# Kernel optimization log

Measured on AMD Instinct MI355X. Metric: run time of the kernel, lower is better.

## Reference

```python
import jax, jax.numpy as jnp
import numpy as np
from jax import lax

NC = 80
REG_MAX = 16
BINS = REG_MAX + 1
RADIUS = 2.5
TOPK = 10
L_BOX, L_CLS, L_DFL = 7.5, 1.0, 1.5


def focal_bce(x, t, alpha=0.25, gamma=2.0):
    # numerically stable BCE-with-logits: max(x,0) - x*t + log1p(exp(-|x|))
    p = jax.nn.sigmoid(x)
    ce = jnp.maximum(x, 0.0) - x * t + jnp.log1p(jnp.exp(-jnp.abs(x)))
    p_t = p * t + (1.0 - p) * (1.0 - t)
    a_t = alpha * t + (1.0 - alpha) * (1.0 - t)
    return ce * a_t * (1.0 - p_t) ** gamma


def _level_loss(reg, cls, boxes, labels, stride):
    B, _, H, W = reg.shape
    HW = H * W
    G = boxes.shape[1]
    gy, gx = jnp.meshgrid(jnp.arange(H, dtype=jnp.float32), jnp.arange(W, dtype=jnp.float32), indexing='ij')
    centers = jnp.stack([gx + 0.5, gy + 0.5], -1).reshape(HW, 2)  # [HW,2]
    gt = boxes / stride  # [B,G,4]
    gctr = (gt[..., :2] + gt[..., 2:]) * 0.5  # [B,G,2]
    cx = centers[None, :, None, 0]
    cy = centers[None, :, None, 1]
    dl = cx - gt[:, None, :, 0]
    dt = cy - gt[:, None, :, 1]
    dr = gt[:, None, :, 2] - cx
    db = gt[:, None, :, 3] - cy
    in_gt = (dl > 0) & (dt > 0) & (dr > 0) & (db > 0)
    in_ctr = ((cx >= gctr[:, None, :, 0] - RADIUS) & (cx <= gctr[:, None, :, 0] + RADIUS)
              & (cy >= gctr[:, None, :, 1] - RADIUS) & (cy <= gctr[:, None, :, 1] + RADIUS))
    mask = in_gt & in_ctr  # [B,HW,G]
    any_pos = jnp.any(mask, axis=(1, 2))  # [B]
    # fallback: topk closest anchor centers per GT (smallest distance along point dim)
    dist = jnp.sqrt(((centers[None, :, None, :] - gctr[:, None, :, :]) ** 2).sum(-1))  # [B,HW,G]
    k = min(TOPK, HW)
    _, idx = lax.top_k(-jnp.swapaxes(dist, 1, 2), k)  # [B,G,k]
    fb = jnp.zeros((B, HW, G), bool).at[jnp.arange(B)[:, None, None], idx, jnp.arange(G)[None, :, None]].set(True)
    mask = jnp.where(any_pos[:, None, None], mask, fb)
    mf = mask.astype(jnp.float32)
    n_pos = mf.sum((1, 2))  # [B] (>=1 by construction of fallback)

    cls_flat = cls.transpose(0, 2, 3, 1).reshape(B, HW, NC)
    reg_flat = reg.transpose(0, 2, 3, 1).reshape(B, HW, 4, BINS)

    # ---- DFL ----
    ltrb = jnp.clip(jnp.stack([dl, dt, dr, db], -1), 0.0)  # [B,HW,G,4]
    tgt = jnp.clip(ltrb, 0.0, REG_MAX - 1e-4)
    lb = jnp.floor(tgt).astype(jnp.int32)
    rb = jnp.minimum(lb + 1, REG_MAX)
    wl = rb.astype(jnp.float32) - tgt
    wr = tgt - lb.astype(jnp.float32)
    logp = jax.nn.log_softmax(reg_flat, -1)  # [B,HW,4,BINS]
    bi = jnp.arange(B)[:, None, None, None]
    pi = jnp.arange(HW)[None, :, None, None]
    ki = jnp.arange(4)[None, None, None, :]
    dfl_pair = -(logp[bi, pi, ki, lb] * wl + logp[bi, pi, ki, rb] * wr)  # [B,HW,G,4]
    dfl = ((dfl_pair * mf[..., None]).sum((1, 2, 3)) / (n_pos * 4.0)).sum()

    # ---- box (IoU, detached as in original) ----
    prob = jax.nn.softmax(reg_flat, -1)
    d = (prob * jnp.arange(BINS, dtype=jnp.float32)).sum(-1)  # [B,HW,4]
    pcx = centers[None, :, 0]
    pcy = centers[None, :, 1]
    pred_box = jnp.stack([pcx - d[..., 0], pcy - d[..., 1], pcx + d[..., 2], pcy + d[..., 3]], -1)  # [B,HW,4]
    b1 = pred_box[:, :, None, :]
    b2 = gt[:, None, :, :]
    iw = jnp.clip(jnp.minimum(b1[..., 2:], b2[..., 2:]) - jnp.maximum(b1[..., :2], b2[..., :2]), 0.0)
    inter = iw[..., 0] * iw[..., 1]
    a1 = (b1[..., 2] - b1[..., 0]) * (b1[..., 3] - b1[..., 1])
    a2 = (b2[..., 2] - b2[..., 0]) * (b2[..., 3] - b2[..., 1])
    iou = lax.stop_gradient(inter / (a1 + a2 - inter + 1e-6))  # [B,HW,G]
    box = ((1.0 - iou) * mf).sum()

    # ---- cls (focal BCE, soft IoU targets). Decompose one-hot target:
    # per positive pair: sum_c f(logit_c,0) - f(logit_cls,0) + f(logit_cls,iou)
    fz = focal_bce(cls_flat, 0.0)  # [B,HW,NC]
    fz_sum = fz.sum(-1)  # [B,HW]
    bi2 = jnp.arange(B)[:, None, None]
    pi2 = jnp.arange(HW)[None, :, None]
    ci = labels[:, None, :]  # [B,1,G]
    cls_at = cls_flat[bi2, pi2, ci]  # [B,HW,G]
    fz_at = fz[bi2, pi2, ci]
    cls_pos = ((fz_sum[:, :, None] - fz_at + focal_bce(cls_at, iou)) * mf).sum()
    pos_pt = jnp.any(mask, -1)  # [B,HW]
    cls_neg = jnp.where(pos_pt, 0.0, fz_sum).sum()
    return box, cls_pos + cls_neg, dfl


def _total(reg0, cls0, reg1, cls1, reg2, cls2, gt_boxes, gt_labels):
    tb = tc = td = 0.0
    for r, c, s in ((reg0, cls0, 8.0), (reg1, cls1, 16.0), (reg2, cls2, 32.0)):
        b, cl, d = _level_loss(r, c, gt_boxes, gt_labels, s)
        tb = tb + b
        tc = tc + cl
        td = td + d
    loss = L_BOX * tb + L_CLS * tc + L_DFL * td
    return loss, tb, tc, td


def setup_inputs() -> dict:
    key = jax.random.key(0)
    ks = jax.random.split(key, 10)
    B, G = 16, 32
    d = {}
    for i, (h, w) in enumerate(((80, 80), (40, 40), (20, 20))):
        d[f'reg{i}'] = jax.random.normal(ks[2 * i], (B, 4 * BINS, h, w), jnp.float32)
        d[f'cls{i}'] = jax.random.normal(ks[2 * i + 1], (B, NC, h, w), jnp.float32)
    ctr = jax.random.uniform(ks[6], (B, G, 2), minval=0.0, maxval=640.0)
    wh = jax.random.uniform(ks[7], (B, G, 2), minval=16.0, maxval=160.0)
    x1y1 = jnp.clip(ctr - wh * 0.5, 0.0, 640.0)
    x2y2 = jnp.clip(ctr + wh * 0.5, 0.0, 640.0)
    d['gt_boxes'] = jnp.concatenate([x1y1, x2y2], -1)
    d['gt_labels'] = jax.random.randint(ks[8], (B, G), 0, NC, jnp.int32)
    return d


def reference(reg0, cls0, reg1, cls1, reg2, cls2, gt_boxes, gt_labels):
    return _total(reg0, cls0, reg1, cls1, reg2, cls2, gt_boxes, gt_labels)
```

## Files before the change

### kernel.cpp

```cpp
#include <hip/hip_runtime.h>
#include <math.h>

#define NCLS 80
#define BINS 17
#define REGMAX 16
#define NG 32
#define NB 16
#define KTOP 10
#define RAD 2.5f

#define PLANE    134400
#define FZP_OFF  256
#define DV_OFF   (256 + 8 * PLANE)
#define LZ_OFF   (256 + 12 * PLANE)
#define WS_NEED  ((size_t)(256 + 16 * PLANE) * 4)
#define NBLOCKS_B (34 * 16)

__device__ __constant__ int c_lvlbase[3] = { 0, 102400, 128000 };

__device__ __forceinline__ float focal0(float x) {
    float e   = __expf(-fabsf(x));
    float inv = 1.0f / (1.0f + e);
    float p   = (x >= 0.0f) ? inv : e * inv;
    float ce  = fmaxf(x, 0.0f) + __logf(1.0f + e);
    return ce * 0.75f * p * p;
}

__device__ __forceinline__ float focal_t(float x, float t) {
    float e   = __expf(-fabsf(x));
    float inv = 1.0f / (1.0f + e);
    float p   = (x >= 0.0f) ? inv : e * inv;
    float ce  = fmaxf(x, 0.0f) - x * t + __logf(1.0f + e);
    float pt  = p * t + (1.0f - p) * (1.0f - t);
    float at  = 0.25f * t + 0.75f * (1.0f - t);
    float om  = 1.0f - pt;
    return ce * at * om * om;
}

__global__ __launch_bounds__(512) void k_stream(
    const float* __restrict__ reg0, const float* __restrict__ cls0,
    const float* __restrict__ reg1, const float* __restrict__ cls1,
    const float* __restrict__ reg2, const float* __restrict__ cls2,
    float* __restrict__ ws)
{
    int id  = blockIdx.x;
    int tid = threadIdx.x;
    if (id < 192) {
        int lvl = id / 64, rem = id % 64, b = rem / 4, k = rem % 4;
        const float* regp = (lvl == 0) ? reg0 : (lvl == 1 ? reg1 : reg2);
        int W  = (lvl == 0) ? 80 : (lvl == 1 ? 40 : 20);
        int HW = W * W;
        const float* base = regp + (size_t)(b * 68 + k * BINS) * HW;
        float sm[16], ex[16];
#pragma unroll
        for (int i = 0; i < 16; ++i) { sm[i] = 0.f; ex[i] = 0.f; }
        for (int t = 0; t < BINS; ++t) {
            const float* rb = base + (size_t)t * HW;
            float tf = (float)t;
#pragma unroll
            for (int j = 0; j < 4; ++j) {
                int p = tid * 4 + 2048 * j;
                if (p < HW) {
                    float4 x = *(const float4*)(rb + p);
                    float e0 = __expf(x.x), e1 = __expf(x.y);
                    float e2 = __expf(x.z), e3 = __expf(x.w);
                    sm[j*4+0] += e0; ex[j*4+0] += e0 * tf;
                    sm[j*4+1] += e1; ex[j*4+1] += e1 * tf;
                    sm[j*4+2] += e2; ex[j*4+2] += e2 * tf;
                    sm[j*4+3] += e3; ex[j*4+3] += e3 * tf;
                }
            }
        }
        int pidx = c_lvlbase[lvl] + b * HW;
#pragma unroll
        for (int j = 0; j < 4; ++j) {
            int p = tid * 4 + 2048 * j;
            if (p < HW) {
                float4 dv4 = make_float4(ex[j*4+0] / sm[j*4+0], ex[j*4+1] / sm[j*4+1],
                                         ex[j*4+2] / sm[j*4+2], ex[j*4+3] / sm[j*4+3]);
                float4 lz4 = make_float4(__logf(sm[j*4+0]), __logf(sm[j*4+1]),
                                         __logf(sm[j*4+2]), __logf(sm[j*4+3]));
                *(float4*)(ws + DV_OFF + (size_t)k * PLANE + pidx + p) = dv4;
                *(float4*)(ws + LZ_OFF + (size_t)k * PLANE + pidx + p) = lz4;
            }
        }
    } else {
        int id2 = id - 192;
        int lvl = id2 / 128, rem = id2 % 128, b = rem / 8, cg = rem % 8;
        const float* clsp = (lvl == 0) ? cls0 : (lvl == 1 ? cls1 : cls2);
        int W  = (lvl == 0) ? 80 : (lvl == 1 ? 40 : 20);
        int HW = W * W;
        const float* base = clsp + (size_t)(b * 80 + cg * 10) * HW;
        float fz[16];
#pragma unroll
        for (int i = 0; i < 16; ++i) fz[i] = 0.f;
        for (int t = 0; t < 10; ++t) {
            const float* rb = base + (size_t)t * HW;
#pragma unroll
            for (int j = 0; j < 4; ++j) {
                int p = tid * 4 + 2048 * j;
                if (p < HW) {
                    float4 x = *(const float4*)(rb + p);
                    fz[j*4+0] += focal0(x.x); fz[j*4+1] += focal0(x.y);
                    fz[j*4+2] += focal0(x.z); fz[j*4+3] += focal0(x.w);
                }
            }
        }
        int pidx = c_lvlbase[lvl] + b * HW;
#pragma unroll
        for (int j = 0; j < 4; ++j) {
            int p = tid * 4 + 2048 * j;
            if (p < HW) {
                *(float4*)(ws + FZP_OFF + (size_t)cg * PLANE + pidx + p) =
                    make_float4(fz[j*4+0], fz[j*4+1], fz[j*4+2], fz[j*4+3]);
            }
        }
    }
}

__global__ __launch_bounds__(256) void k_finish(
    const float* __restrict__ reg0, const float* __restrict__ cls0,
    const float* __restrict__ reg1, const float* __restrict__ cls1,
    const float* __restrict__ reg2, const float* __restrict__ cls2,
    const float* __restrict__ gtb,  const int* __restrict__ lab,
    float* __restrict__ ws, float* __restrict__ out)
{
    float* acc  = ws;
    float* npos = ws + 8;
    float* dfln = ws + 56;
    int*   cnt  = (int*)(ws + 152);

    int bx = blockIdx.x;
    int b  = blockIdx.y;
    int lvl, tix, W; const float *regp, *clsp; float inv_s;
    if (bx < 25)      { lvl = 0; tix = bx;      W = 80; regp = reg0; clsp = cls0; inv_s = 0.125f;   }
    else if (bx < 32) { lvl = 1; tix = bx - 25; W = 40; regp = reg1; clsp = cls1; inv_s = 0.0625f;  }
    else              { lvl = 2; tix = bx - 32; W = 20; regp = reg2; clsp = cls2; inv_s = 0.03125f; }
    int HW = W * W;
    int tile = tix * 256;

    int tid  = threadIdx.x;
    int lane = tid & 63;
    int w    = tid >> 6;
    int pt   = tile + tid;
    bool v   = pt < HW;
    int pidx = c_lvlbase[lvl] + b * HW + (v ? pt : 0);

    __shared__ float s_bx[NG][6];
    __shared__ int   s_lab[NG];
    __shared__ int   s_any, s_tick, s_fb[NG][KTOP];
    __shared__ float red[4][4];

    if (tid == 0) s_any = 0;
    if (tid < NG) {
        int g = tid;
        float4 bb4 = *(const float4*)(gtb + (b * NG + g) * 4);
        float x1 = bb4.x * inv_s, y1 = bb4.y * inv_s;
        float x2 = bb4.z * inv_s, y2 = bb4.w * inv_s;
        s_bx[g][0] = x1; s_bx[g][1] = y1; s_bx[g][2] = x2; s_bx[g][3] = y2;
        s_bx[g][4] = (x1 + x2) * 0.5f; s_bx[g][5] = (y1 + y2) * 0.5f;
        s_lab[g] = lab[b * NG + g];
    }
    __syncthreads();

    {
        int g = tid >> 3, wi = tid & 7;
        float x1 = s_bx[g][0], y1 = s_bx[g][1];
        float x2 = s_bx[g][2], y2 = s_bx[g][3];
        float gcx = s_bx[g][4], gcy = s_bx[g][5];
        int jc = (int)floorf(gcx), ic = (int)floorf(gcy);
        bool any = false;
#pragma unroll
        for (int r = 0; r < 11; ++r) {
            int ci = wi + 8 * r;
            if (ci < 81) {
                int j = jc + (ci % 9) - 4, i = ic + (ci / 9) - 4;
                if (j >= 0 && j < W && i >= 0 && i < W) {
                    float cx = (float)j + 0.5f, cy = (float)i + 0.5f;
                    bool m = (cx - x1 > 0.0f) && (cy - y1 > 0.0f) &&
                             (x2 - cx > 0.0f) && (y2 - cy > 0.0f) &&
                             (cx >= gcx - RAD) && (cx <= gcx + RAD) &&
                             (cy >= gcy - RAD) && (cy <= gcy + RAD);
                    any = any || m;
                }
            }
        }
        if (__any(any) && lane == 0) atomicOr(&s_any, 1);
    }
    __syncthreads();
    bool anyb = s_any != 0;

    if (!anyb) {
        if (tid < NG) {
            int g = tid;
            float gcx = s_bx[g][4], gcy = s_bx[g][5];
            float bd[KTOP]; int bi[KTOP];
            for (int t = 0; t < KTOP; ++t) { bd[t] = 3.0e38f; bi[t] = 0; }
            for (int p = 0; p < HW; ++p) {
                float cx = (float)(p % W) + 0.5f;
                float cy = (float)(p / W) + 0.5f;
                float dx = cx - gcx, dy = cy - gcy;
                float d = dx * dx + dy * dy;
                if (d < bd[KTOP - 1]) {
                    int t = KTOP - 1;
                    while (t > 0 && d < bd[t - 1]) { bd[t] = bd[t-1]; bi[t] = bi[t-1]; --t; }
                    bd[t] = d; bi[t] = p;
                }
            }
            for (int t = 0; t < KTOP; ++t) s_fb[g][t] = bi[t];
        }
        __syncthreads();
    }

    float fz = 0.f;
    if (v) {
#pragma unroll
        for (int cg = 0; cg < 8; ++cg)
            fz += ws[FZP_OFF + (size_t)cg * PLANE + pidx];
    }

    float bxa = 0.f, cla = 0.f, dfa = 0.f, np = 0.f;
    bool pos = false, ld = false;
    float dv0 = 0, dv1 = 0, dv2 = 0, dv3 = 0, lzv[4] = {0, 0, 0, 0};
    int ri = v ? pt / W : 0;
    float cy = (float)ri + 0.5f;
    float cx = (float)(pt - ri * W) + 0.5f;

    if (v) {
        for (int g = 0; g < NG; ++g) {
            float x1 = s_bx[g][0], y1 = s_bx[g][1];
            float x2 = s_bx[g][2], y2 = s_bx[g][3];
            float dl = cx - x1, dt = cy - y1, dr = x2 - cx, db = y2 - cy;
            bool mk;
            if (anyb) {
                float gx = s_bx[g][4], gy = s_bx[g][5];
                mk = (dl > 0.f) && (dt > 0.f) && (dr > 0.f) && (db > 0.f) &&
                     (cx >= gx - RAD) && (cx <= gx + RAD) &&
                     (cy >= gy - RAD) && (cy <= gy + RAD);
            } else {
                mk = false;
                for (int t = 0; t < KTOP; ++t) mk = mk || (s_fb[g][t] == pt);
            }
            if (mk) {
                pos = true;
                np += 1.f;
                if (!ld) {
                    dv0 = ws[DV_OFF + 0 * PLANE + pidx];
                    dv1 = ws[DV_OFF + 1 * PLANE + pidx];
                    dv2 = ws[DV_OFF + 2 * PLANE + pidx];
                    dv3 = ws[DV_OFF + 3 * PLANE + pidx];
#pragma unroll
                    for (int k = 0; k < 4; ++k)
                        lzv[k] = ws[LZ_OFF + (size_t)k * PLANE + pidx];
                    ld = true;
                }
                float px1 = cx - dv0, py1 = cy - dv1;
                float px2 = cx + dv2, py2 = cy + dv3;
                float pa = (px2 - px1) * (py2 - py1);
                float ix1 = fmaxf(px1, x1), iy1 = fmaxf(py1, y1);
                float ix2 = fminf(px2, x2), iy2 = fminf(py2, y2);
                float iw = fmaxf(ix2 - ix1, 0.f), ih = fmaxf(iy2 - iy1, 0.f);
                float inter = iw * ih;
                float ga = (x2 - x1) * (y2 - y1);
                float iou = inter / (pa + ga - inter + 1e-6f);
                bxa += 1.f - iou;
                float ltrb[4] = { dl, dt, dr, db };
#pragma unroll
                for (int k = 0; k < 4; ++k) {
                    float tt = fminf(fmaxf(ltrb[k], 0.f), 15.9999f);
                    float lf = floorf(tt); int lb = (int)lf;
                    int rb = lb + 1 > REGMAX ? REGMAX : lb + 1;
                    float wl = (float)rb - tt, wr = tt - lf;
                    float xl = regp[(size_t)(b * 68 + k * BINS + lb) * HW + pt];
                    float xr = regp[(size_t)(b * 68 + k * BINS + rb) * HW + pt];
                    dfa -= (xl - lzv[k]) * wl + (xr - lzv[k]) * wr;
                }
                int cc = s_lab[g];
                float xat = clsp[(size_t)(b * 80 + cc) * HW + pt];
                cla += fz - focal0(xat) + focal_t(xat, iou);
            }
        }
        if (!pos) cla += fz;
    }

    float v0 = bxa, v1 = cla, v2 = dfa, v3 = np;
    for (int off = 32; off > 0; off >>= 1) {
        v0 += __shfl_down(v0, off);
        v1 += __shfl_down(v1, off);
        v2 += __shfl_down(v2, off);
        v3 += __shfl_down(v3, off);
    }
    if (lane == 0) { red[w][0] = v0; red[w][1] = v1; red[w][2] = v2; red[w][3] = v3; }
    __syncthreads();
    if (tid == 0) {
        float t0 = 0, t1 = 0, t2 = 0, t3 = 0;
        for (int wv = 0; wv < 4; ++wv) {
            t0 += red[wv][0]; t1 += red[wv][1]; t2 += red[wv][2]; t3 += red[wv][3];
        }
        atomicAdd(&acc[0], t0);
        atomicAdd(&acc[1], t1);
        atomicAdd(&dfln[lvl * NB + b], t2);
        atomicAdd(&npos[lvl * NB + b], t3);
    }

    if (tid == 0) {
        __threadfence();
        s_tick = atomicAdd(cnt, 1);
    }
    __syncthreads();
    if (s_tick == NBLOCKS_B - 1 && tid < 64) {
        float vs = 0.f;
        if (lane < 48) {
            float n = atomicAdd(&npos[lane], 0.0f);
            float d = atomicAdd(&dfln[lane], 0.0f);
            if (n > 0.f) vs = d / (n * 4.0f);
        }
        for (int off = 32; off > 0; off >>= 1) vs += __shfl_down(vs, off);
        if (lane == 0) {
            float tbv = atomicAdd(&acc[0], 0.0f);
            float tcv = atomicAdd(&acc[1], 0.0f);
            out[0] = 7.5f * tbv + tcv + 1.5f * vs;
            out[1] = tbv; out[2] = tcv; out[3] = vs;
        }
    }
}

__global__ __launch_bounds__(512, 2) void k_main_fb(
    const float* __restrict__ reg0, const float* __restrict__ cls0,
    const float* __restrict__ reg1, const float* __restrict__ cls1,
    const float* __restrict__ reg2, const float* __restrict__ cls2,
    const float* __restrict__ gtb,  const int* __restrict__ lab,
    float* __restrict__ acc, float* __restrict__ npos, float* __restrict__ dfln,
    int* __restrict__ cnt, float* __restrict__ out)
{
    int bx = blockIdx.x;
    int b  = blockIdx.y;
    int lvl, tix, W; const float *regp, *clsp; float inv_s;
    if (bx < 25)      { lvl = 0; tix = bx;      W = 80; regp = reg0; clsp = cls0; inv_s = 0.125f;   }
    else if (bx < 32) { lvl = 1; tix = bx - 25; W = 40; regp = reg1; clsp = cls1; inv_s = 0.0625f;  }
    else              { lvl = 2; tix = bx - 32; W = 20; regp = reg2; clsp = cls2; inv_s = 0.03125f; }
    int HW = W * W;
    int tile = tix * 256;
    int tid  = threadIdx.x;
    int lane = tid & 63;
    int w    = tid >> 6;
    int p0   = tile + 4 * lane;
    bool v   = p0 < HW;
    int pb   = v ? p0 : HW - 4;

    __shared__ float s_bx[NG][6];
    __shared__ int   s_lab[NG];
    __shared__ float s_dv[4][256], s_lz[4][256], s_fzp[4][256], s_fzs[256];
    __shared__ unsigned char s_ps[8][64];
    __shared__ float red[8][4];
    __shared__ int   s_any, s_tick, s_fb[NG][KTOP];

    if (tid == 0) s_any = 0;
    if (tid < NG) {
        int g = tid;
        float4 bb4 = *(const float4*)(gtb + (b * NG + g) * 4);
        float x1 = bb4.x * inv_s, y1 = bb4.y * inv_s;
        float x2 = bb4.z * inv_s, y2 = bb4.w * inv_s;
        s_bx[g][0] = x1; s_bx[g][1] = y1; s_bx[g][2] = x2; s_bx[g][3] = y2;
        s_bx[g][4] = (x1 + x2) * 0.5f; s_bx[g][5] = (y1 + y2) * 0.5f;
        s_lab[g] = lab[b * NG + g];
    }
    __syncthreads();
    {
        int g = tid >> 4, wi = tid & 15;
        float x1 = s_bx[g][0], y1 = s_bx[g][1];
        float x2 = s_bx[g][2], y2 = s_bx[g][3];
        float gcx = s_bx[g][4], gcy = s_bx[g][5];
        int jc = (int)floorf(gcx), ic = (int)floorf(gcy);
        bool any = false;
#pragma unroll
        for (int r = 0; r < 6; ++r) {
            int ci = wi + 16 * r;
            if (ci < 81) {
                int j = jc + (ci % 9) - 4, i = ic + (ci / 9) - 4;
                if (j >= 0 && j < W && i >= 0 && i < W) {
                    float cx = (float)j + 0.5f, cy = (float)i + 0.5f;
                    bool m = (cx - x1 > 0.0f) && (cy - y1 > 0.0f) &&
                             (x2 - cx > 0.0f) && (y2 - cy > 0.0f) &&
                             (cx >= gcx - RAD) && (cx <= gcx + RAD) &&
                             (cy >= gcy - RAD) && (cy <= gcy + RAD);
                    any = any || m;
                }
            }
        }
        if (__any(any) && lane == 0) atomicOr(&s_any, 1);
    }
    __syncthreads();
    bool anyb = s_any != 0;
    if (!anyb) {
        if (tid < NG) {
            int g = tid;
            float gcx = s_bx[g][4], gcy = s_bx[g][5];
            float bd[KTOP]; int bi[KTOP];
            for (int t = 0; t < KTOP; ++t) { bd[t] = 3.0e38f; bi[t] = 0; }
            for (int p = 0; p < HW; ++p) {
                float cx = (float)(p % W) + 0.5f;
                float cy = (float)(p / W) + 0.5f;
                float dx = cx - gcx, dy = cy - gcy;
                float d = dx * dx + dy * dy;
                if (d < bd[KTOP - 1]) {
                    int t = KTOP - 1;
                    while (t > 0 && d < bd[t - 1]) { bd[t] = bd[t-1]; bi[t] = bi[t-1]; --t; }
                    bd[t] = d; bi[t] = p;
                }
            }
            for (int t = 0; t < KTOP; ++t) s_fb[g][t] = bi[t];
        }
        __syncthreads();
    }
    if (w < 4) {
        const float* bp = regp + (size_t)(b * 68 + w * BINS) * HW + pb;
        float m[4], sm[4], ex[4];
#pragma unroll
        for (int j = 0; j < 4; ++j) { m[j] = -3.0e38f; sm[j] = 0.f; ex[j] = 0.f; }
#pragma unroll
        for (int t = 0; t < BINS; ++t) {
            float4 x4 = *(const float4*)(bp + (size_t)t * HW);
            float xv[4] = { x4.x, x4.y, x4.z, x4.w };
#pragma unroll
            for (int j = 0; j < 4; ++j) {
                float nm = fmaxf(m[j], xv[j]);
                float a  = __expf(m[j] - nm);
                float bb = __expf(xv[j] - nm);
                sm[j] = sm[j] * a + bb;
                ex[j] = ex[j] * a + bb * (float)t;
                m[j]  = nm;
            }
        }
        *(float4*)&s_dv[w][4 * lane] =
            make_float4(ex[0] / sm[0], ex[1] / sm[1], ex[2] / sm[2], ex[3] / sm[3]);
        *(float4*)&s_lz[w][4 * lane] =
            make_float4(__logf(sm[0]) + m[0], __logf(sm[1]) + m[1],
                        __logf(sm[2]) + m[2], __logf(sm[3]) + m[3]);
    } else {
        int q = w - 4;
        const float* bp = clsp + (size_t)(b * 80 + q * 20) * HW + pb;
        float fz[4] = { 0.f, 0.f, 0.f, 0.f };
#pragma unroll
        for (int t = 0; t < 20; ++t) {
            float4 c4 = *(const float4*)(bp + (size_t)t * HW);
            fz[0] += focal0(c4.x); fz[1] += focal0(c4.y);
            fz[2] += focal0(c4.z); fz[3] += focal0(c4.w);
        }
        *(float4*)&s_fzp[q][4 * lane] = make_float4(fz[0], fz[1], fz[2], fz[3]);
    }
    __syncthreads();
    if (tid < 256)
        s_fzs[tid] = s_fzp[0][tid] + s_fzp[1][tid] + s_fzp[2][tid] + s_fzp[3][tid];
    __syncthreads();

    float bxa = 0.f, cla = 0.f, dfa = 0.f, np = 0.f;
    unsigned posm = 0;
    int ri = p0 / W;
    float cy  = (float)ri + 0.5f;
    float cxb = (float)(p0 - ri * W) + 0.5f;
    if (v) {
        int r0 = tile / W, r1 = min(tile + 255, HW - 1) / W;
        float cyLo = (float)r0 + 0.5f, cyHi = (float)r1 + 0.5f;
#pragma unroll
        for (int gi = 0; gi < 4; ++gi) {
            int g = w + 8 * gi;
            float x1 = s_bx[g][0], y1 = s_bx[g][1];
            float x2 = s_bx[g][2], y2 = s_bx[g][3];
            float gx = s_bx[g][4], gy = s_bx[g][5];
            if (anyb) {
                if (!((cyHi > y1) && (y2 > cyLo) &&
                      (cyHi >= gy - RAD) && (cyLo <= gy + RAD))) continue;
            }
#pragma unroll
            for (int j = 0; j < 4; ++j) {
                float cx = cxb + (float)j;
                float dl = cx - x1, dt = cy - y1, dr = x2 - cx, db = y2 - cy;
                bool mk;
                if (anyb) {
                    mk = (dl > 0.f) && (dt > 0.f) && (dr > 0.f) && (db > 0.f) &&
                         (cx >= gx - RAD) && (cx <= gx + RAD) &&
                         (cy >= gy - RAD) && (cy <= gy + RAD);
                } else {
                    int pt = p0 + j;
                    mk = false;
                    for (int t = 0; t < KTOP; ++t) mk = mk || (s_fb[g][t] == pt);
                }
                if (mk) {
                    posm |= (1u << j);
                    np += 1.f;
                    int ptl = 4 * lane + j, pt = p0 + j;
                    float dv0 = s_dv[0][ptl], dv1 = s_dv[1][ptl];
                    float dv2 = s_dv[2][ptl], dv3 = s_dv[3][ptl];
                    float px1 = cx - dv0, py1 = cy - dv1;
                    float px2 = cx + dv2, py2 = cy + dv3;
                    float pa = (px2 - px1) * (py2 - py1);
                    float ix1 = fmaxf(px1, x1), iy1 = fmaxf(py1, y1);
                    float ix2 = fminf(px2, x2), iy2 = fminf(py2, y2);
                    float iw = fmaxf(ix2 - ix1, 0.f), ih = fmaxf(iy2 - iy1, 0.f);
                    float inter = iw * ih;
                    float ga = (x2 - x1) * (y2 - y1);
                    float iou = inter / (pa + ga - inter + 1e-6f);
                    bxa += 1.f - iou;
                    float ltrb[4] = { dl, dt, dr, db };
#pragma unroll
                    for (int k = 0; k < 4; ++k) {
                        float tt = fminf(fmaxf(ltrb[k], 0.f), 15.9999f);
                        float lf = floorf(tt); int lb = (int)lf;
                        int rb = lb + 1 > REGMAX ? REGMAX : lb + 1;
                        float wl = (float)rb - tt, wr = tt - lf;
                        float lzk = s_lz[k][ptl];
                        float xl = regp[(size_t)(b * 68 + k * BINS + lb) * HW + pt];
                        float xr = regp[(size_t)(b * 68 + k * BINS + rb) * HW + pt];
                        dfa -= (xl - lzk) * wl + (xr - lzk) * wr;
                    }
                    int cc = s_lab[g];
                    float xat = clsp[(size_t)(b * 80 + cc) * HW + pt];
                    cla += s_fzs[ptl] - focal0(xat) + focal_t(xat, iou);
                }
            }
        }
    }
    s_ps[w][lane] = (unsigned char)posm;
    __syncthreads();
    if (tid < 256 && tile + tid < HW) {
        unsigned pg = 0;
#pragma unroll
        for (int wv = 0; wv < 8; ++wv) pg |= s_ps[wv][tid >> 2];
        if (!((pg >> (tid & 3)) & 1u)) cla += s_fzs[tid];
    }
    float v0 = bxa, v1 = cla, v2 = dfa, v3 = np;
    for (int off = 32; off > 0; off >>= 1) {
        v0 += __shfl_down(v0, off);
        v1 += __shfl_down(v1, off);
        v2 += __shfl_down(v2, off);
        v3 += __shfl_down(v3, off);
    }
    if (lane == 0) { red[w][0] = v0; red[w][1] = v1; red[w][2] = v2; red[w][3] = v3; }
    __syncthreads();
    if (tid == 0) {
        float t0 = 0, t1 = 0, t2 = 0, t3 = 0;
        for (int wv = 0; wv < 8; ++wv) {
            t0 += red[wv][0]; t1 += red[wv][1]; t2 += red[wv][2]; t3 += red[wv][3];
        }
        atomicAdd(&acc[0], t0);
        atomicAdd(&acc[1], t1);
        atomicAdd(&dfln[lvl * NB + b], t2);
        atomicAdd(&npos[lvl * NB + b], t3);
    }
    if (tid == 0) {
        __threadfence();
        s_tick = atomicAdd(cnt, 1);
    }
    __syncthreads();
    if (s_tick == NBLOCKS_B - 1 && tid < 64) {
        float vs = 0.f;
        if (lane < 48) {
            float n = atomicAdd(&npos[lane], 0.0f);
            float d = atomicAdd(&dfln[lane], 0.0f);
            if (n > 0.f) vs = d / (n * 4.0f);
        }
        for (int off = 32; off > 0; off >>= 1) vs += __shfl_down(vs, off);
        if (lane == 0) {
            float tbv = atomicAdd(&acc[0], 0.0f);
            float tcv = atomicAdd(&acc[1], 0.0f);
            out[0] = 7.5f * tbv + tcv + 1.5f * vs;
            out[1] = tbv; out[2] = tcv; out[3] = vs;
        }
    }
}

extern "C" void kernel_launch(void* const* d_in, const int* in_sizes, int n_in,
                              void* d_out, int out_size, void* d_ws, size_t ws_size,
                              hipStream_t stream) {
    const float* reg0 = (const float*)d_in[0];
    const float* cls0 = (const float*)d_in[1];
    const float* reg1 = (const float*)d_in[2];
    const float* cls1 = (const float*)d_in[3];
    const float* reg2 = (const float*)d_in[4];
    const float* cls2 = (const float*)d_in[5];
    const float* gtb  = (const float*)d_in[6];
    const int*   lab  = (const int*)d_in[7];
    float* out = (float*)d_out;
    float* ws  = (float*)d_ws;

    hipMemsetAsync(d_ws, 0, 612, stream);
    if (ws_size >= WS_NEED) {
        k_stream<<<576, 512, 0, stream>>>(reg0, cls0, reg1, cls1, reg2, cls2, ws);
        k_finish<<<dim3(34, NB), 256, 0, stream>>>(reg0, cls0, reg1, cls1, reg2, cls2,
                                                   gtb, lab, ws, out);
    } else {
        k_main_fb<<<dim3(34, NB), 512, 0, stream>>>(reg0, cls0, reg1, cls1, reg2, cls2,
                                                    gtb, lab,
                                                    ws, ws + 8, ws + 56,
                                                    (int*)(ws + 152), out);
    }
}
```

Baseline: 71.74 us.

## Rework streaming kernel into wave-granular work items with grid-stride scheduling

The reduction kernel now assigns each 64-lane wave a small work item (one 256-pixel chunk of one reg side or one 20-class cls group) and loops over items with a grid stride. Previously each 512-thread block handled a whole plane slice, which left level-1/2 blocks mostly idle. Class partial sums drop from 8 groups to 4, which shrinks workspace and the reads in the finish kernel. The new layout gives better load balance and occupancy, at the cost of fewer pixels per thread and slightly more index math.

After: 102.9 us. 1.43x slower.

```diff
diff --git a/kernel.cpp b/kernel.cpp
--- a/kernel.cpp
+++ b/kernel.cpp
@@ -11,10 +11,11 @@
 
 #define PLANE    134400
 #define FZP_OFF  256
-#define DV_OFF   (256 + 8 * PLANE)
-#define LZ_OFF   (256 + 12 * PLANE)
-#define WS_NEED  ((size_t)(256 + 16 * PLANE) * 4)
+#define DV_OFF   (256 + 4 * PLANE)
+#define LZ_OFF   (256 + 8 * PLANE)
+#define WS_NEED  ((size_t)(256 + 12 * PLANE) * 4)
 #define NBLOCKS_B (34 * 16)
+#define NITEMS   (3200 + 896 + 256)
 
 __device__ __constant__ int c_lvlbase[3] = { 0, 102400, 128000 };
 
@@ -37,83 +38,63 @@
     return ce * at * om * om;
 }
 
-__global__ __launch_bounds__(512) void k_stream(
+__global__ __launch_bounds__(256, 8) void k_stream(
     const float* __restrict__ reg0, const float* __restrict__ cls0,
     const float* __restrict__ reg1, const float* __restrict__ cls1,
     const float* __restrict__ reg2, const float* __restrict__ cls2,
     float* __restrict__ ws)
 {
-    int id  = blockIdx.x;
-    int tid = threadIdx.x;
-    if (id < 192) {
-        int lvl = id / 64, rem = id % 64, b = rem / 4, k = rem % 4;
-        const float* regp = (lvl == 0) ? reg0 : (lvl == 1 ? reg1 : reg2);
-        int W  = (lvl == 0) ? 80 : (lvl == 1 ? 40 : 20);
+    int w_in = threadIdx.x >> 6, lane = threadIdx.x & 63;
+    int gw = blockIdx.x * 4 + w_in;
+    int nw = gridDim.x * 4;
+    for (int it = gw; it < NITEMS; it += nw) {
+        int lvl, rem;
+        if (it < 3200)      { lvl = 0; rem = it; }
+        else if (it < 4096) { lvl = 1; rem = it - 3200; }
+        else                { lvl = 2; rem = it - 4096; }
+        int ck = (lvl == 0) ? 25 : ((lvl == 1) ? 7 : 2);
+        int W  = (lvl == 0) ? 80 : ((lvl == 1) ? 40 : 20);
         int HW = W * W;
-        const float* base = regp + (size_t)(b * 68 + k * BINS) * HW;
-        float sm[16], ex[16];
-#pragma unroll
-        for (int i = 0; i < 16; ++i) { sm[i] = 0.f; ex[i] = 0.f; }
-        for (int t = 0; t < BINS; ++t) {
-            const float* rb = base + (size_t)t * HW;
-            float tf = (float)t;
-#pragma unroll
-            for (int j = 0; j < 4; ++j) {
-                int p = tid * 4 + 2048 * j;
-                if (p < HW) {
-                    float4 x = *(const float4*)(rb + p);
-                    float e0 = __expf(x.x), e1 = __expf(x.y);
-                    float e2 = __expf(x.z), e3 = __expf(x.w);
-                    sm[j*4+0] += e0; ex[j*4+0] += e0 * tf;
-                    sm[j*4+1] += e1; ex[j*4+1] += e1 * tf;
-                    sm[j*4+2] += e2; ex[j*4+2] += e2 * tf;
-                    sm[j*4+3] += e3; ex[j*4+3] += e3 * tf;
-                }
-            }
-        }
-        int pidx = c_lvlbase[lvl] + b * HW;
-#pragma unroll
-        for (int j = 0; j < 4; ++j) {
-            int p = tid * 4 + 2048 * j;
-            if (p < HW) {
-                float4 dv4 = make_float4(ex[j*4+0] / sm[j*4+0], ex[j*4+1] / sm[j*4+1],
-                                         ex[j*4+2] / sm[j*4+2], ex[j*4+3] / sm[j*4+3]);
-                float4 lz4 = make_float4(__logf(sm[j*4+0]), __logf(sm[j*4+1]),
-                                         __logf(sm[j*4+2]), __logf(sm[j*4+3]));
-                *(float4*)(ws + DV_OFF + (size_t)k * PLANE + pidx + p) = dv4;
-                *(float4*)(ws + LZ_OFF + (size_t)k * PLANE + pidx + p) = lz4;
-            }
-        }
-    } else {
-        int id2 = id - 192;
-        int lvl = id2 / 128, rem = id2 % 128, b = rem / 8, cg = rem % 8;
-        const float* clsp = (lvl == 0) ? cls0 : (lvl == 1 ? cls1 : cls2);
-        int W  = (lvl == 0) ? 80 : (lvl == 1 ? 40 : 20);
-        int HW = W * W;
-        const float* base = clsp + (size_t)(b * 80 + cg * 10) * HW;
-        float fz[16];
-#pragma unroll
-        for (int i = 0; i < 16; ++i) fz[i] = 0.f;
-        for (int t = 0; t < 10; ++t) {
-            const float* rb = base + (size_t)t * HW;
-#pragma unroll
-            for (int j = 0; j < 4; ++j) {
-                int p = tid * 4 + 2048 * j;
-                if (p < HW) {
-                    float4 x = *(const float4*)(rb + p);
-                    fz[j*4+0] += focal0(x.x); fz[j*4+1] += focal0(x.y);
-                    fz[j*4+2] += focal0(x.z); fz[j*4+3] += focal0(x.w);
-                }
-            }
-        }
-        int pidx = c_lvlbase[lvl] + b * HW;
-#pragma unroll
-        for (int j = 0; j < 4; ++j) {
-            int p = tid * 4 + 2048 * j;
-            if (p < HW) {
-                *(float4*)(ws + FZP_OFF + (size_t)cg * PLANE + pidx + p) =
-                    make_float4(fz[j*4+0], fz[j*4+1], fz[j*4+2], fz[j*4+3]);
-            }
+        const float* regp = (lvl == 0) ? reg0 : ((lvl == 1) ? reg1 : reg2);
+        const float* clsp = (lvl == 0) ? cls0 : ((lvl == 1) ? cls1 : cls2);
+        int per_b = 8 * ck;
+        int b  = rem / per_b, r2 = rem % per_b;
+        int u  = r2 / ck,     c  = r2 % ck;
+        int p0 = c * 256 + 4 * lane;
+        bool v = p0 < HW;
+        int pb = v ? p0 : HW - 4;
+        int pidx = c_lvlbase[lvl] + b * HW + p0;
+        if (u < 4) {
+            const float* base = regp + (size_t)(b * 68 + u * BINS) * HW + pb;
+            float sm0 = 0, sm1 = 0, sm2 = 0, sm3 = 0;
+            float e0 = 0, e1 = 0, e2 = 0, e3 = 0;
+#pragma unroll
+            for (int t = 0; t < BINS; ++t) {
+                float4 x = *(const float4*)(base + (size_t)t * HW);
+                float a0 = __expf(x.x), a1 = __expf(x.y);
+                float a2 = __expf(x.z), a3 = __expf(x.w);
+                float tf = (float)t;
+                sm0 += a0; e0 += a0 * tf; sm1 += a1; e1 += a1 * tf;
+                sm2 += a2; e2 += a2 * tf; sm3 += a3; e3 += a3 * tf;
+            }
+            if (v) {
+                *(float4*)(ws + DV_OFF + (size_t)u * PLANE + pidx) =
+                    make_float4(e0 / sm0, e1 / sm1, e2 / sm2, e3 / sm3);
+                *(float4*)(ws + LZ_OFF + (size_t)u * PLANE + pidx) =
+                    make_float4(__logf(sm0), __logf(sm1), __logf(sm2), __logf(sm3));
+            }
+        } else {
+            int q = u - 4;
+            const float* base = clsp + (size_t)(b * 80 + q * 20) * HW + pb;
+            float f0 = 0, f1 = 0, f2 = 0, f3 = 0;
+#pragma unroll
+            for (int t = 0; t < 20; ++t) {
+                float4 x = *(const float4*)(base + (size_t)t * HW);
+                f0 += focal0(x.x); f1 += focal0(x.y);
+                f2 += focal0(x.z); f3 += focal0(x.w);
+            }
+            if (v) *(float4*)(ws + FZP_OFF + (size_t)q * PLANE + pidx) =
+                       make_float4(f0, f1, f2, f3);
         }
     }
 }
@@ -215,7 +196,7 @@
     float fz = 0.f;
     if (v) {
 #pragma unroll
-        for (int cg = 0; cg < 8; ++cg)
+        for (int cg = 0; cg < 4; ++cg)
             fz += ws[FZP_OFF + (size_t)cg * PLANE + pidx];
     }
 
@@ -586,7 +567,7 @@
 
     hipMemsetAsync(d_ws, 0, 612, stream);
     if (ws_size >= WS_NEED) {
-        k_stream<<<576, 512, 0, stream>>>(reg0, cls0, reg1, cls1, reg2, cls2, ws);
+        k_stream<<<1088, 256, 0, stream>>>(reg0, cls0, reg1, cls1, reg2, cls2, ws);
         k_finish<<<dim3(34, NB), 256, 0, stream>>>(reg0, cls0, reg1, cls1, reg2, cls2,
                                                    gtb, lab, ws, out);
     } else {
```
